# Optimization experiments

Measured on AMD Instinct MI355X. Metric: run time of the kernel, lower is better.

The kernel has to match this reference:

```python
import jax, jax.numpy as jnp
import numpy as np

B, S, D, VOCAB = 64, 2048, 256, 32000


def setup_inputs() -> dict:
    key = jax.random.key(0)
    k1, k2, k3 = jax.random.split(key, 3)
    chunk = jax.random.randint(k1, (B, S), 0, VOCAB, dtype=jnp.int32)
    encoding = jax.random.normal(k2, (B, S, D), dtype=jnp.float32)
    # idf weights are positive; uniform (0,1] avoids zero-sum pathologies
    idf = jax.random.uniform(k3, (VOCAB,), dtype=jnp.float32, minval=1e-3, maxval=1.0)
    return {"chunk": chunk, "encoding": encoding, "idf": idf}


def reference(chunk, encoding, idf):
    """Batched, fused version of DocumentDualEmbedder.get_doc_embedding.

    chunk:    [B, S] int token ids
    encoding: [B, S, D] transformer outputs
    idf:      [vocab] idf weight table
    returns:  [B, 4*D] (idf-weighted mean | max | min | std)
    """
    seq_len = encoding.shape[1]
    w = idf[chunk]                                  # [B, S] gather
    w = w / jnp.sum(w, axis=1, keepdims=True)       # per-doc normalize
    mean_emb = jnp.einsum('bs,bsd->bd', w, encoding)
    max_emb = jnp.max(encoding, axis=1)
    min_emb = jnp.min(encoding, axis=1)
    # torch.std default: unbiased (divide by S-1)
    mu = jnp.mean(encoding, axis=1, keepdims=True)  # [B, 1, D]
    var = jnp.sum(jnp.square(encoding - mu), axis=1) / (seq_len - 1)
    std_emb = jnp.sqrt(var)
    return jnp.concatenate([mean_emb, max_emb, min_emb, std_emb], axis=-1)
```

## Files before the change

### kernel.cpp

```cpp
#include <hip/hip_runtime.h>

#define BB 64
#define SS 2048
#define DD 256
#define NSPLIT 32
#define S_PER (SS / NSPLIT)

__global__ __launch_bounds__(256) void wsum_kernel(
    const int* __restrict__ chunk, const float* __restrict__ idf,
    float* __restrict__ wsum) {
  int b = blockIdx.x;
  int tid = threadIdx.x;
  float s = 0.f;
  for (int i = tid; i < SS; i += 256) s += idf[chunk[b * SS + i]];
  __shared__ float red[256];
  red[tid] = s;
  __syncthreads();
  for (int off = 128; off > 0; off >>= 1) {
    if (tid < off) red[tid] += red[tid + off];
    __syncthreads();
  }
  if (tid == 0) wsum[b] = red[0];
}

__global__ __launch_bounds__(256) void partial_kernel(
    const int* __restrict__ chunk, const float* __restrict__ enc,
    const float* __restrict__ idf, float* __restrict__ pswe,
    float* __restrict__ pse, float* __restrict__ pse2,
    float* __restrict__ pmx, float* __restrict__ pmn) {
  int split = blockIdx.x;
  int b = blockIdx.y;
  int tid = threadIdx.x;
  int dg = tid & 63;
  int ssub = tid >> 6;
  int s0 = split * S_PER;

  __shared__ float sw[S_PER];
  if (tid < S_PER) sw[tid] = idf[chunk[b * SS + s0 + tid]];
  __syncthreads();

  float swe[4] = {0.f, 0.f, 0.f, 0.f};
  float se[4] = {0.f, 0.f, 0.f, 0.f};
  float se2[4] = {0.f, 0.f, 0.f, 0.f};
  float mx[4], mn[4];
#pragma unroll
  for (int k = 0; k < 4; k++) {
    mx[k] = -3.4028234e38f;
    mn[k] = 3.4028234e38f;
  }

  const float* base = enc + ((size_t)(b * SS + s0)) * DD + (size_t)dg * 4;
#pragma unroll 4
  for (int i = 0; i < S_PER / 4; i++) {
    int srel = ssub + 4 * i;
    float w = sw[srel];
    float4 e = *(const float4*)(base + (size_t)srel * DD);
    float ev[4] = {e.x, e.y, e.z, e.w};
#pragma unroll
    for (int k = 0; k < 4; k++) {
      swe[k] = fmaf(w, ev[k], swe[k]);
      se[k] += ev[k];
      se2[k] = fmaf(ev[k], ev[k], se2[k]);
      mx[k] = fmaxf(mx[k], ev[k]);
      mn[k] = fminf(mn[k], ev[k]);
    }
  }

  __shared__ float red[5][4][DD];
#pragma unroll
  for (int k = 0; k < 4; k++) {
    red[0][ssub][dg * 4 + k] = swe[k];
    red[1][ssub][dg * 4 + k] = se[k];
    red[2][ssub][dg * 4 + k] = se2[k];
    red[3][ssub][dg * 4 + k] = mx[k];
    red[4][ssub][dg * 4 + k] = mn[k];
  }
  __syncthreads();

  int d = tid;
  size_t gbase = ((size_t)b * NSPLIT + split) * DD + d;
  pswe[gbase] = (red[0][0][d] + red[0][1][d]) + (red[0][2][d] + red[0][3][d]);
  pse[gbase] = (red[1][0][d] + red[1][1][d]) + (red[1][2][d] + red[1][3][d]);
  pse2[gbase] = (red[2][0][d] + red[2][1][d]) + (red[2][2][d] + red[2][3][d]);
  pmx[gbase] = fmaxf(fmaxf(red[3][0][d], red[3][1][d]),
                     fmaxf(red[3][2][d], red[3][3][d]));
  pmn[gbase] = fminf(fminf(red[4][0][d], red[4][1][d]),
                     fminf(red[4][2][d], red[4][3][d]));
}

__global__ __launch_bounds__(256) void final_kernel(
    const float* __restrict__ pswe, const float* __restrict__ pse,
    const float* __restrict__ pse2, const float* __restrict__ pmx,
    const float* __restrict__ pmn, const float* __restrict__ wsum,
    float* __restrict__ out) {
  int b = blockIdx.x;
  int d = threadIdx.x;
  float swe = 0.f, se = 0.f, se2 = 0.f;
  float mx = -3.4028234e38f, mn = 3.4028234e38f;
  for (int sp = 0; sp < NSPLIT; sp++) {
    size_t idx = ((size_t)b * NSPLIT + sp) * DD + d;
    swe += pswe[idx];
    se += pse[idx];
    se2 += pse2[idx];
    mx = fmaxf(mx, pmx[idx]);
    mn = fminf(mn, pmn[idx]);
  }
  float mean_w = swe / wsum[b];
  float mu = se / (float)SS;
  float var = (se2 - (float)SS * mu * mu) / (float)(SS - 1);
  float stdv = sqrtf(fmaxf(var, 0.f));
  size_t ob = (size_t)b * 4 * DD;
  out[ob + d] = mean_w;
  out[ob + DD + d] = mx;
  out[ob + 2 * DD + d] = mn;
  out[ob + 3 * DD + d] = stdv;
}

extern "C" void kernel_launch(void* const* d_in, const int* in_sizes, int n_in,
                              void* d_out, int out_size, void* d_ws,
                              size_t ws_size, hipStream_t stream) {
  const int* chunk = (const int*)d_in[0];
  const float* enc = (const float*)d_in[1];
  const float* idf = (const float*)d_in[2];
  float* out = (float*)d_out;

  float* ws = (float*)d_ws;
  size_t n = (size_t)BB * NSPLIT * DD;
  float* pswe = ws;
  float* pse = ws + n;
  float* pse2 = ws + 2 * n;
  float* pmx = ws + 3 * n;
  float* pmn = ws + 4 * n;
  float* wsum = ws + 5 * n;

  wsum_kernel<<<BB, 256, 0, stream>>>(chunk, idf, wsum);
  partial_kernel<<<dim3(NSPLIT, BB), 256, 0, stream>>>(chunk, enc, idf, pswe,
                                                       pse, pse2, pmx, pmn);
  final_kernel<<<BB, DD, 0, stream>>>(pswe, pse, pse2, pmx, pmn, wsum, out);
}
```

Measured before the change: 210.8 us.

## Fuse idf weight-sum into partial kernel and parallelize final reduction

Removes the separate wsum kernel launch by having each partial block reduce its 64 gathered idf weights with a wavefront shuffle and write one per-split sum, which the final kernel then totals. The final kernel now uses 1024 threads per batch row, splitting the NSPLIT partials across four groups and combining them through shared memory, and each thread writes one output element. The main loop unroll also goes from 4 to 8. The goal is to cut one launch and the serial latency of the final pass, at the cost of more shared memory and a larger block in the final kernel.

```diff
diff --git a/kernel.cpp b/kernel.cpp
--- a/kernel.cpp
+++ b/kernel.cpp
@@ -6,28 +6,14 @@
 #define NSPLIT 32
 #define S_PER (SS / NSPLIT)
 
-__global__ __launch_bounds__(256) void wsum_kernel(
-    const int* __restrict__ chunk, const float* __restrict__ idf,
-    float* __restrict__ wsum) {
-  int b = blockIdx.x;
-  int tid = threadIdx.x;
-  float s = 0.f;
-  for (int i = tid; i < SS; i += 256) s += idf[chunk[b * SS + i]];
-  __shared__ float red[256];
-  red[tid] = s;
-  __syncthreads();
-  for (int off = 128; off > 0; off >>= 1) {
-    if (tid < off) red[tid] += red[tid + off];
-    __syncthreads();
-  }
-  if (tid == 0) wsum[b] = red[0];
-}
+#define FLT_BIG 3.4028234e38f
 
 __global__ __launch_bounds__(256) void partial_kernel(
     const int* __restrict__ chunk, const float* __restrict__ enc,
     const float* __restrict__ idf, float* __restrict__ pswe,
     float* __restrict__ pse, float* __restrict__ pse2,
-    float* __restrict__ pmx, float* __restrict__ pmn) {
+    float* __restrict__ pmx, float* __restrict__ pmn,
+    float* __restrict__ pws) {
   int split = blockIdx.x;
   int b = blockIdx.y;
   int tid = threadIdx.x;
@@ -39,18 +25,25 @@
   if (tid < S_PER) sw[tid] = idf[chunk[b * SS + s0 + tid]];
   __syncthreads();
 
+  if (tid < 64) {
+    float w = sw[tid];
+#pragma unroll
+    for (int off = 32; off > 0; off >>= 1) w += __shfl_down(w, off, 64);
+    if (tid == 0) pws[b * NSPLIT + split] = w;
+  }
+
   float swe[4] = {0.f, 0.f, 0.f, 0.f};
   float se[4] = {0.f, 0.f, 0.f, 0.f};
   float se2[4] = {0.f, 0.f, 0.f, 0.f};
   float mx[4], mn[4];
 #pragma unroll
   for (int k = 0; k < 4; k++) {
-    mx[k] = -3.4028234e38f;
-    mn[k] = 3.4028234e38f;
+    mx[k] = -FLT_BIG;
+    mn[k] = FLT_BIG;
   }
 
   const float* base = enc + ((size_t)(b * SS + s0)) * DD + (size_t)dg * 4;
-#pragma unroll 4
+#pragma unroll 8
   for (int i = 0; i < S_PER / 4; i++) {
     int srel = ssub + 4 * i;
     float w = sw[srel];
@@ -88,16 +81,21 @@
                      fminf(red[4][2][d], red[4][3][d]));
 }
 
-__global__ __launch_bounds__(256) void final_kernel(
+__global__ __launch_bounds__(1024) void final_kernel(
     const float* __restrict__ pswe, const float* __restrict__ pse,
     const float* __restrict__ pse2, const float* __restrict__ pmx,
-    const float* __restrict__ pmn, const float* __restrict__ wsum,
+    const float* __restrict__ pmn, const float* __restrict__ pws,
     float* __restrict__ out) {
   int b = blockIdx.x;
-  int d = threadIdx.x;
+  int tid = threadIdx.x;
+  int d = tid & 255;
+  int grp = tid >> 8;
+
   float swe = 0.f, se = 0.f, se2 = 0.f;
-  float mx = -3.4028234e38f, mn = 3.4028234e38f;
-  for (int sp = 0; sp < NSPLIT; sp++) {
+  float mx = -FLT_BIG, mn = FLT_BIG;
+#pragma unroll
+  for (int j = 0; j < NSPLIT / 4; j++) {
+    int sp = grp * (NSPLIT / 4) + j;
     size_t idx = ((size_t)b * NSPLIT + sp) * DD + d;
     swe += pswe[idx];
     se += pse[idx];
@@ -105,15 +103,47 @@
     mx = fmaxf(mx, pmx[idx]);
     mn = fminf(mn, pmn[idx]);
   }
-  float mean_w = swe / wsum[b];
-  float mu = se / (float)SS;
-  float var = (se2 - (float)SS * mu * mu) / (float)(SS - 1);
-  float stdv = sqrtf(fmaxf(var, 0.f));
-  size_t ob = (size_t)b * 4 * DD;
-  out[ob + d] = mean_w;
-  out[ob + DD + d] = mx;
-  out[ob + 2 * DD + d] = mn;
-  out[ob + 3 * DD + d] = stdv;
+
+  __shared__ float red[5][4][DD];
+  red[0][grp][d] = swe;
+  red[1][grp][d] = se;
+  red[2][grp][d] = se2;
+  red[3][grp][d] = mx;
+  red[4][grp][d] = mn;
+
+  __shared__ float wsp[NSPLIT];
+  __shared__ float wtot_s;
+  if (tid < NSPLIT) wsp[tid] = pws[b * NSPLIT + tid];
+  __syncthreads();
+  if (tid == 0) {
+    float t = 0.f;
+#pragma unroll
+    for (int i = 0; i < NSPLIT; i++) t += wsp[i];
+    wtot_s = t;
+  }
+  __syncthreads();
+
+  float cswe = (red[0][0][d] + red[0][1][d]) + (red[0][2][d] + red[0][3][d]);
+  float cse = (red[1][0][d] + red[1][1][d]) + (red[1][2][d] + red[1][3][d]);
+  float cse2 = (red[2][0][d] + red[2][1][d]) + (red[2][2][d] + red[2][3][d]);
+  float cmx = fmaxf(fmaxf(red[3][0][d], red[3][1][d]),
+                    fmaxf(red[3][2][d], red[3][3][d]));
+  float cmn = fminf(fminf(red[4][0][d], red[4][1][d]),
+                    fminf(red[4][2][d], red[4][3][d]));
+
+  int stat = tid >> 8;
+  float val;
+  if (stat == 0) {
+    val = cswe / wtot_s;
+  } else if (stat == 1) {
+    val = cmx;
+  } else if (stat == 2) {
+    val = cmn;
+  } else {
+    float mu = cse / (float)SS;
+    val = sqrtf(fmaxf((cse2 - (float)SS * mu * mu) / (float)(SS - 1), 0.f));
+  }
+  out[(size_t)b * 4 * DD + tid] = val;
 }
 
 extern "C" void kernel_launch(void* const* d_in, const int* in_sizes, int n_in,
@@ -131,10 +161,10 @@
   float* pse2 = ws + 2 * n;
   float* pmx = ws + 3 * n;
   float* pmn = ws + 4 * n;
-  float* wsum = ws + 5 * n;
+  float* pws = ws + 5 * n;
 
-  wsum_kernel<<<BB, 256, 0, stream>>>(chunk, idf, wsum);
   partial_kernel<<<dim3(NSPLIT, BB), 256, 0, stream>>>(chunk, enc, idf, pswe,
-                                                       pse, pse2, pmx, pmn);
-  final_kernel<<<BB, DD, 0, stream>>>(pswe, pse, pse2, pmx, pmn, wsum, out);
+                                                       pse, pse2, pmx, pmn,
+                                                       pws);
+  final_kernel<<<BB, 1024, 0, stream>>>(pswe, pse, pse2, pmx, pmn, pws, out);
 }
```

Result: faster. 201.7 us (-4.3%).

## Fuse weight-sum, partial and final reductions into one kernel with last-block atomic

Applied to the files above, without the earlier changes.

Merges the three kernels into one. Each split block computes its own idf weight partial sum with a wavefront shuffle, and the last block per batch row, found through an atomic counter, does the cross-split reduction and writes the output. This removes two kernel launches and the separate pass over chunk/idf, but adds a memset launch and threadfence/atomic overhead, and the final reduction runs on only 64 blocks at the tail. The encoding loop unroll is also raised from 4 to 8.

```diff
diff --git a/kernel.cpp b/kernel.cpp
--- a/kernel.cpp
+++ b/kernel.cpp
@@ -6,28 +6,15 @@
 #define NSPLIT 32
 #define S_PER (SS / NSPLIT)
 
-__global__ __launch_bounds__(256) void wsum_kernel(
-    const int* __restrict__ chunk, const float* __restrict__ idf,
-    float* __restrict__ wsum) {
-  int b = blockIdx.x;
-  int tid = threadIdx.x;
-  float s = 0.f;
-  for (int i = tid; i < SS; i += 256) s += idf[chunk[b * SS + i]];
-  __shared__ float red[256];
-  red[tid] = s;
-  __syncthreads();
-  for (int off = 128; off > 0; off >>= 1) {
-    if (tid < off) red[tid] += red[tid + off];
-    __syncthreads();
-  }
-  if (tid == 0) wsum[b] = red[0];
-}
+#define FLT_BIG 3.4028234e38f
 
-__global__ __launch_bounds__(256) void partial_kernel(
+__global__ __launch_bounds__(256) void fused_kernel(
     const int* __restrict__ chunk, const float* __restrict__ enc,
     const float* __restrict__ idf, float* __restrict__ pswe,
     float* __restrict__ pse, float* __restrict__ pse2,
-    float* __restrict__ pmx, float* __restrict__ pmn) {
+    float* __restrict__ pmx, float* __restrict__ pmn,
+    float* __restrict__ pws, unsigned int* __restrict__ cnt,
+    float* __restrict__ out) {
   int split = blockIdx.x;
   int b = blockIdx.y;
   int tid = threadIdx.x;
@@ -39,18 +26,25 @@
   if (tid < S_PER) sw[tid] = idf[chunk[b * SS + s0 + tid]];
   __syncthreads();
 
+  if (tid < 64) {
+    float w = sw[tid];
+#pragma unroll
+    for (int off = 32; off > 0; off >>= 1) w += __shfl_down(w, off, 64);
+    if (tid == 0) pws[b * NSPLIT + split] = w;
+  }
+
   float swe[4] = {0.f, 0.f, 0.f, 0.f};
   float se[4] = {0.f, 0.f, 0.f, 0.f};
   float se2[4] = {0.f, 0.f, 0.f, 0.f};
   float mx[4], mn[4];
 #pragma unroll
   for (int k = 0; k < 4; k++) {
-    mx[k] = -3.4028234e38f;
-    mn[k] = 3.4028234e38f;
+    mx[k] = -FLT_BIG;
+    mn[k] = FLT_BIG;
   }
 
   const float* base = enc + ((size_t)(b * SS + s0)) * DD + (size_t)dg * 4;
-#pragma unroll 4
+#pragma unroll 8
   for (int i = 0; i < S_PER / 4; i++) {
     int srel = ssub + 4 * i;
     float w = sw[srel];
@@ -86,33 +80,39 @@
                      fmaxf(red[3][2][d], red[3][3][d]));
   pmn[gbase] = fminf(fminf(red[4][0][d], red[4][1][d]),
                      fminf(red[4][2][d], red[4][3][d]));
-}
 
-__global__ __launch_bounds__(256) void final_kernel(
-    const float* __restrict__ pswe, const float* __restrict__ pse,
-    const float* __restrict__ pse2, const float* __restrict__ pmx,
-    const float* __restrict__ pmn, const float* __restrict__ wsum,
-    float* __restrict__ out) {
-  int b = blockIdx.x;
-  int d = threadIdx.x;
-  float swe = 0.f, se = 0.f, se2 = 0.f;
-  float mx = -3.4028234e38f, mn = 3.4028234e38f;
+  __shared__ int sIsLast;
+  __syncthreads();
+  if (tid == 0) {
+    __threadfence();
+    unsigned int old = atomicAdd(&cnt[b], 1u);
+    sIsLast = (old == NSPLIT - 1);
+  }
+  __syncthreads();
+  if (!sIsLast) return;
+  __threadfence();
+
+  float cswe = 0.f, cse = 0.f, cse2 = 0.f;
+  float cmx = -FLT_BIG, cmn = FLT_BIG;
+  float wtot = 0.f;
+#pragma unroll 4
   for (int sp = 0; sp < NSPLIT; sp++) {
     size_t idx = ((size_t)b * NSPLIT + sp) * DD + d;
-    swe += pswe[idx];
-    se += pse[idx];
-    se2 += pse2[idx];
-    mx = fmaxf(mx, pmx[idx]);
-    mn = fminf(mn, pmn[idx]);
+    cswe += pswe[idx];
+    cse += pse[idx];
+    cse2 += pse2[idx];
+    cmx = fmaxf(cmx, pmx[idx]);
+    cmn = fminf(cmn, pmn[idx]);
+    wtot += pws[b * NSPLIT + sp];
   }
-  float mean_w = swe / wsum[b];
-  float mu = se / (float)SS;
-  float var = (se2 - (float)SS * mu * mu) / (float)(SS - 1);
-  float stdv = sqrtf(fmaxf(var, 0.f));
+
+  float mu = cse / (float)SS;
+  float stdv =
+      sqrtf(fmaxf((cse2 - (float)SS * mu * mu) / (float)(SS - 1), 0.f));
   size_t ob = (size_t)b * 4 * DD;
-  out[ob + d] = mean_w;
-  out[ob + DD + d] = mx;
-  out[ob + 2 * DD + d] = mn;
+  out[ob + d] = cswe / wtot;
+  out[ob + DD + d] = cmx;
+  out[ob + 2 * DD + d] = cmn;
   out[ob + 3 * DD + d] = stdv;
 }
 
@@ -131,10 +131,11 @@
   float* pse2 = ws + 2 * n;
   float* pmx = ws + 3 * n;
   float* pmn = ws + 4 * n;
-  float* wsum = ws + 5 * n;
+  float* pws = ws + 5 * n;
+  unsigned int* cnt = (unsigned int*)(ws + 5 * n + 4096);
 
-  wsum_kernel<<<BB, 256, 0, stream>>>(chunk, idf, wsum);
-  partial_kernel<<<dim3(NSPLIT, BB), 256, 0, stream>>>(chunk, enc, idf, pswe,
-                                                       pse, pse2, pmx, pmn);
-  final_kernel<<<BB, DD, 0, stream>>>(pswe, pse, pse2, pmx, pmn, wsum, out);
+  hipMemsetAsync(cnt, 0, BB * sizeof(unsigned int), stream);
+
+  fused_kernel<<<dim3(NSPLIT, BB), 256, 0, stream>>>(
+      chunk, enc, idf, pswe, pse, pse2, pmx, pmn, pws, cnt, out);
 }
```

After: 340.1 us. +61.3%, slower.
